# Optimization experiments

Measured on AMD Instinct MI355X. Metric: run time of the kernel, lower is better.

## Reference

```python
import jax, jax.numpy as jnp
import numpy as np

N_AGENTS = 32
STATE_DIM = 6 * N_AGENTS      # 192
CONTROL_DIM = 3 * N_AGENTS    # 96
HIDDEN = 100
NEWTON_ITERS = 40

# Index maps from the cvxpy objective:
#   p[u_x_r]^T u[u_idx] + p[u_y_r]^T u[2*u_idx] + p[u_z_r]^T u[3*u_idx]
_u_idx = np.arange(N_AGENTS)
P_IDX = np.concatenate([3 * np.arange(1, N_AGENTS + 1),
                        4 * np.arange(1, N_AGENTS + 1),
                        5 * np.arange(1, N_AGENTS + 1)])
U_IDX = np.concatenate([_u_idx, 2 * _u_idx, 3 * _u_idx])


def _p_net(t, z, W1, b1, W2, b2, W3, b3):
    # DefaultPNet: MLP on concat([t, z]) with tanh hiddens (hidden_dim=100)
    x = jnp.concatenate([t, z], axis=-1)          # [B, 1+STATE_DIM]
    h = jnp.tanh(x @ W1 + b1)
    h = jnp.tanh(h @ W2 + b2)
    return h @ W3 + b3                            # [B, STATE_DIM]


def _solve_qp(q):
    # min_u q^T u + 0.5||u||^2 + 0.25||u||^4  (unconstrained, strictly convex)
    # Stationarity: q + (1+||u||^2) u = 0 => u = -q/(1+s), s = ||u||^2
    # => s (1+s)^2 = ||q||^2 ; solve scalar cubic per row via Newton.
    r = jnp.sum(q * q, axis=-1)                   # [B]
    s0 = jnp.cbrt(r)                              # good init: s ~ r^(1/3) for large r

    def step(s, _):
        one = 1.0 + s
        f = s * one * one - r
        fp = one * one + 2.0 * s * one
        return jnp.maximum(s - f / fp, 0.0), None

    s, _ = jax.lax.scan(step, s0, None, length=NEWTON_ITERS)
    return -q / (1.0 + s)[:, None]                # [B, CONTROL_DIM]


def setup_inputs() -> dict:
    key = jax.random.key(0)
    ks = jax.random.split(key, 8)
    B = 131072
    in_dim = 1 + STATE_DIM
    sc1 = 1.0 / np.sqrt(in_dim)
    sc2 = 1.0 / np.sqrt(HIDDEN)
    return {
        "z": jax.random.normal(ks[0], (B, STATE_DIM), jnp.float32),
        "t": jax.random.uniform(ks[1], (B, 1), jnp.float32),
        "W1": jax.random.normal(ks[2], (in_dim, HIDDEN), jnp.float32) * sc1,
        "b1": jnp.zeros((HIDDEN,), jnp.float32),
        "W2": jax.random.normal(ks[3], (HIDDEN, HIDDEN), jnp.float32) * sc2,
        "b2": jnp.zeros((HIDDEN,), jnp.float32),
        "W3": jax.random.normal(ks[4], (HIDDEN, STATE_DIM), jnp.float32) * sc2,
        "b3": jnp.zeros((STATE_DIM,), jnp.float32),
    }


def reference(z, t, W1, b1, W2, b2, W3, b3):
    p = _p_net(t, z, W1, b1, W2, b2, W3, b3)      # [B, STATE_DIM]
    # Accumulate linear coefficients onto u (indices overlap, so scatter-add)
    q = jnp.zeros((p.shape[0], CONTROL_DIM), p.dtype).at[:, U_IDX].add(p[:, P_IDX])
    return _solve_qp(q)                            # ustar [B, CONTROL_DIM]
```

## Files before the change

kernel.cpp:

```cpp
#include <hip/hip_runtime.h>
#include <hip/hip_bf16.h>


typedef __attribute__((ext_vector_type(8))) short short8;
typedef __attribute__((ext_vector_type(4))) short short4v;
typedef __attribute__((ext_vector_type(4))) float f32x4;

#define HST 116

__device__ __forceinline__ unsigned short f2bf(float f) {
  unsigned u = __float_as_uint(f);
  u += 0x7fffu + ((u >> 16) & 1u);
  return (unsigned short)(u >> 16);
}
__device__ __forceinline__ float tanh_fast(float x) {
  float ax = fabsf(x);
  float e = __builtin_amdgcn_exp2f(ax * -2.88539008177792681f);
  float r = (1.f - e) * __builtin_amdgcn_rcpf(1.f + e);
  return copysignf(r, x);
}

__global__ void cvx_prep(const float* __restrict__ W1, const float* __restrict__ b1,
                         const float* __restrict__ W2, const float* __restrict__ b2,
                         const float* __restrict__ W3, const float* __restrict__ b3,
                         short* __restrict__ pw) {
  int idx = blockIdx.x * 256 + threadIdx.x;

  if (idx < 21504) {
    int kt = idx / 3584, rem = idx % 3584;
    int nt = rem / 512, e = rem % 512;
    int lane = e >> 3, j = e & 7;
    int k = kt * 32 + (lane >> 4) * 8 + j;
    int n = nt * 16 + (lane & 15);
    float wv = (n < 100) ? W1[(k + 1) * 100 + n] : 0.f;
    pw[(kt * 7 + nt) * 512 + e] = (short)f2bf(wv);
    return;
  }
  idx -= 21504;
  if (idx < 14336) {
    int kt = idx / 3584, rem = idx % 3584;
    int nt = rem / 512, e = rem % 512;
    int lane = e >> 3, j = e & 7;
    int k = kt * 32 + (lane >> 4) * 8 + j;
    int n = nt * 16 + (lane & 15);
    float wv = (k < 100 && n < 100) ? W2[k * 100 + n] : 0.f;
    pw[21504 + (kt * 7 + nt) * 512 + e] = (short)f2bf(wv);
    return;
  }
  idx -= 14336;
  if (idx < 12288) {
    int kt = idx / 3072, rem = idx % 3072;
    int nt = rem / 512, e = rem % 512;
    int lane = e >> 3, j = e & 7;
    int k = kt * 32 + (lane >> 4) * 8 + j;
    int u = nt * 16 + (lane & 15);
    float wv = 0.f;
    if (k < 100) {
      const float* wr = W3 + k * 192;
      if (u <= 31) wv += wr[3 * u + 3];
      if ((u & 1) == 0 && u <= 62) wv += wr[2 * u + 4];
      if (u % 3 == 0 && u <= 93) wv += wr[(5 * u) / 3 + 5];
    }
    pw[35840 + (kt * 6 + nt) * 512 + e] = (short)f2bf(wv);
    return;
  }
  idx -= 12288;
  float* cb = (float*)(pw + 48128);
  if (idx < 112) { cb[idx] = (idx < 100) ? W1[idx] : 0.f; return; }
  idx -= 112;
  if (idx < 112) { cb[112 + idx] = (idx < 100) ? b1[idx] : 0.f; return; }
  idx -= 112;
  if (idx < 112) { cb[224 + idx] = (idx < 100) ? b2[idx] : 0.f; return; }
  idx -= 112;
  if (idx < 96) {
    int u = idx;
    float v = 0.f;
    if (u <= 31) v += b3[3 * u + 3];
    if ((u & 1) == 0 && u <= 62) v += b3[2 * u + 4];
    if (u % 3 == 0 && u <= 93) v += b3[(5 * u) / 3 + 5];
    cb[336 + u] = v;
  }
}

__global__ __launch_bounds__(512, 2) void cvx_main(
    const float* __restrict__ zin, const float* __restrict__ tin,
    const short* __restrict__ pw, float* __restrict__ out) {
  __shared__ __align__(16) short wbuf[48128];
  __shared__ __align__(16) short hbuf[8 * 32 * HST];

  const int tid = threadIdx.x;
  const int wid = tid >> 6;
  const int lane = tid & 63;
  const int l15 = lane & 15;
  const int qd = lane >> 4;

  for (int f = wid; f < 94; f += 8) {
    const short* g = pw + f * 512 + lane * 8;
    __builtin_amdgcn_global_load_lds(
        (const __attribute__((address_space(1))) void*)g,
        (__attribute__((address_space(3))) void*)&wbuf[f * 512], 16, 0, 0);
  }

  const float* cb = (const float*)(pw + 48128);
  float w0v[7], b1v[7], b2v[7], bqv[6];
#pragma unroll
  for (int nt = 0; nt < 7; nt++) {
    w0v[nt] = cb[nt * 16 + l15];
    b1v[nt] = cb[112 + nt * 16 + l15];
    b2v[nt] = cb[224 + nt * 16 + l15];
  }
#pragma unroll
  for (int nt = 0; nt < 6; nt++) bqv[nt] = cb[336 + nt * 16 + l15];

  const int row0 = blockIdx.x * 512 + wid * 32;
  const int hb = wid * 32 * HST;

  f32x4 zc[2][6][2];
  float tc[2];
#pragma unroll
  for (int mt = 0; mt < 2; mt++) {
    const float* zr = zin + (size_t)(row0 + mt * 16 + l15) * 192 + qd * 8;
#pragma unroll
    for (int kt = 0; kt < 6; kt++) {
      zc[mt][kt][0] = *(const f32x4*)(zr + kt * 32);
      zc[mt][kt][1] = *(const f32x4*)(zr + kt * 32 + 4);
    }
    tc[mt] = tin[row0 + mt * 16 + l15];
  }

  __syncthreads();

  auto ldh = [&](int off) -> short8 {
    short4v a = *(const short4v*)&hbuf[off];
    short4v b = *(const short4v*)&hbuf[off + 4];
    return __builtin_shufflevector(a, b, 0, 1, 2, 3, 4, 5, 6, 7);
  };

#pragma unroll 1
  for (int it = 0; it < 2; ++it) {
    const int rb = row0 + it * 256;

    short8 XA[2][6];
#pragma unroll
    for (int mt = 0; mt < 2; mt++)
#pragma unroll
      for (int kt = 0; kt < 6; kt++) {
        union { short8 s; __hip_bfloat162 h[4]; } u;
        f32x4 a = zc[mt][kt][0], b = zc[mt][kt][1];
        u.h[0] = __float22bfloat162_rn(make_float2(a[0], a[1]));
        u.h[1] = __float22bfloat162_rn(make_float2(a[2], a[3]));
        u.h[2] = __float22bfloat162_rn(make_float2(b[0], b[1]));
        u.h[3] = __float22bfloat162_rn(make_float2(b[2], b[3]));
        XA[mt][kt] = u.s;
      }
    float tv0 = tc[0], tv1 = tc[1];

    if (it == 0) {
#pragma unroll
      for (int mt = 0; mt < 2; mt++) {
        const float* zr = zin + (size_t)(row0 + 256 + mt * 16 + l15) * 192 + qd * 8;
#pragma unroll
        for (int kt = 0; kt < 6; kt++) {
          zc[mt][kt][0] = *(const f32x4*)(zr + kt * 32);
          zc[mt][kt][1] = *(const f32x4*)(zr + kt * 32 + 4);
        }
        tc[mt] = tin[row0 + 256 + mt * 16 + l15];
      }
    }

    f32x4 acc[2][7];
#pragma unroll
    for (int nt = 0; nt < 7; nt++) {
      f32x4 zzz = {0.f, 0.f, 0.f, 0.f};
      acc[0][nt] = zzz; acc[1][nt] = zzz;
    }
#pragma unroll
    for (int kt = 0; kt < 6; kt++)
#pragma unroll
      for (int nt = 0; nt < 7; nt++) {
        short8 bf = *(const short8*)&wbuf[(kt * 7 + nt) * 512 + lane * 8];
        acc[0][nt] = __builtin_amdgcn_mfma_f32_16x16x32_bf16(XA[0][kt], bf, acc[0][nt], 0, 0, 0);
        acc[1][nt] = __builtin_amdgcn_mfma_f32_16x16x32_bf16(XA[1][kt], bf, acc[1][nt], 0, 0, 0);
      }
    float tr[2][4];
#pragma unroll
    for (int r = 0; r < 4; r++) {
      tr[0][r] = __shfl(tv0, qd * 4 + r);
      tr[1][r] = __shfl(tv1, qd * 4 + r);
    }
#pragma unroll
    for (int mt = 0; mt < 2; mt++)
#pragma unroll
      for (int nt = 0; nt < 7; nt++)
#pragma unroll
        for (int r = 0; r < 4; r++) {
          float v = fmaf(tr[mt][r], w0v[nt], acc[mt][nt][r] + b1v[nt]);
          hbuf[hb + (mt * 16 + qd * 4 + r) * HST + nt * 16 + l15] = (short)f2bf(tanh_fast(v));
        }

    short8 HA[2][4];
#pragma unroll
    for (int mt = 0; mt < 2; mt++) {
      int ro = hb + (mt * 16 + l15) * HST;
#pragma unroll
      for (int kt = 0; kt < 3; kt++) HA[mt][kt] = ldh(ro + kt * 32 + qd * 8);
      HA[mt][3] = ldh(ro + 96 + (qd & 1) * 8);
    }
#pragma unroll
    for (int nt = 0; nt < 7; nt++) {
      f32x4 zzz = {0.f, 0.f, 0.f, 0.f};
      acc[0][nt] = zzz; acc[1][nt] = zzz;
    }
#pragma unroll
    for (int kt = 0; kt < 4; kt++)
#pragma unroll
      for (int nt = 0; nt < 7; nt++) {
        short8 bf = *(const short8*)&wbuf[(42 + kt * 7 + nt) * 512 + lane * 8];
        acc[0][nt] = __builtin_amdgcn_mfma_f32_16x16x32_bf16(HA[0][kt], bf, acc[0][nt], 0, 0, 0);
        acc[1][nt] = __builtin_amdgcn_mfma_f32_16x16x32_bf16(HA[1][kt], bf, acc[1][nt], 0, 0, 0);
      }
#pragma unroll
    for (int mt = 0; mt < 2; mt++)
#pragma unroll
      for (int nt = 0; nt < 7; nt++)
#pragma unroll
        for (int r = 0; r < 4; r++) {
          float v = acc[mt][nt][r] + b2v[nt];
          hbuf[hb + (mt * 16 + qd * 4 + r) * HST + nt * 16 + l15] = (short)f2bf(tanh_fast(v));
        }

#pragma unroll
    for (int mt = 0; mt < 2; mt++) {
      int ro = hb + (mt * 16 + l15) * HST;
#pragma unroll
      for (int kt = 0; kt < 3; kt++) HA[mt][kt] = ldh(ro + kt * 32 + qd * 8);
      HA[mt][3] = ldh(ro + 96 + (qd & 1) * 8);
    }
    f32x4 qa[2][6];
#pragma unroll
    for (int nt = 0; nt < 6; nt++) {
      f32x4 zzz = {0.f, 0.f, 0.f, 0.f};
      qa[0][nt] = zzz; qa[1][nt] = zzz;
    }
#pragma unroll
    for (int kt = 0; kt < 4; kt++)
#pragma unroll
      for (int nt = 0; nt < 6; nt++) {
        short8 bf = *(const short8*)&wbuf[(70 + kt * 6 + nt) * 512 + lane * 8];
        qa[0][nt] = __builtin_amdgcn_mfma_f32_16x16x32_bf16(HA[0][kt], bf, qa[0][nt], 0, 0, 0);
        qa[1][nt] = __builtin_amdgcn_mfma_f32_16x16x32_bf16(HA[1][kt], bf, qa[1][nt], 0, 0, 0);
      }

#pragma unroll
    for (int mt = 0; mt < 2; mt++) {
#pragma unroll
      for (int nt = 0; nt < 6; nt++) {
        float bq = bqv[nt];
        qa[mt][nt][0] += bq; qa[mt][nt][1] += bq;
        qa[mt][nt][2] += bq; qa[mt][nt][3] += bq;
      }
      f32x4 rs = {0.f, 0.f, 0.f, 0.f};
#pragma unroll
      for (int nt = 0; nt < 6; nt++) rs += qa[mt][nt] * qa[mt][nt];
      float rv[4];
#pragma unroll
      for (int r = 0; r < 4; r++) {
        float v = rs[r];
        v += __shfl_xor(v, 1);
        v += __shfl_xor(v, 2);
        v += __shfl_xor(v, 4);
        v += __shfl_xor(v, 8);
        rv[r] = v;
      }
      float r2 = rv[l15 & 3];
      float s = __builtin_amdgcn_exp2f(__builtin_amdgcn_logf(r2) * 0.333333333333f);
#pragma unroll
      for (int itn = 0; itn < 8; itn++) {
        float one = 1.f + s;
        float fv = fmaf(s * one, one, -r2);
        float fp = one * fmaf(2.f, s, one);
        s = fmaxf(s - fv * __builtin_amdgcn_rcpf(fp), 0.f);
      }
      float myinv = -__builtin_amdgcn_rcpf(1.f + s);
#pragma unroll
      for (int r = 0; r < 4; r++) {
        float inv = __shfl(myinv, (lane & 48) | r);
        float* orow = out + (size_t)(rb + mt * 16 + qd * 4 + r) * 96;
#pragma unroll
        for (int nt = 0; nt < 6; nt++)
          orow[nt * 16 + l15] = qa[mt][nt][r] * inv;
      }
    }
  }
}

extern "C" void kernel_launch(void* const* d_in, const int* in_sizes, int n_in,
                              void* d_out, int out_size, void* d_ws, size_t ws_size,
                              hipStream_t stream) {
  const float* z  = (const float*)d_in[0];
  const float* t  = (const float*)d_in[1];
  const float* W1 = (const float*)d_in[2];
  const float* b1 = (const float*)d_in[3];
  const float* W2 = (const float*)d_in[4];
  const float* b2 = (const float*)d_in[5];
  const float* W3 = (const float*)d_in[6];
  const float* b3 = (const float*)d_in[7];
  float* out = (float*)d_out;
  int B = in_sizes[0] / 192;

  short* pw = (short*)d_ws;
  cvx_prep<<<190, 256, 0, stream>>>(W1, b1, W2, b2, W3, b3, pw);
  cvx_main<<<B / 512, 512, 0, stream>>>(z, t, pw, out);
}
```

Before: 192.8 us.

## Halve rows per wave and double block size to 1024 threads

Each wave now processes one 16-row M tile per iteration instead of two. The block doubles to 16 waves, so each block still covers 512 rows. Bias and W1 time-column vectors move from per-lane registers into a shared LDS array. The aim is to cut register pressure and put more waves on each CU to hide MFMA, LDS and global latency. The cost is that every weight fragment read from LDS now feeds one MFMA instead of two, which doubles LDS weight traffic per unit of work.

```diff
diff --git a/kernel.cpp b/kernel.cpp
--- a/kernel.cpp
+++ b/kernel.cpp
@@ -82,11 +82,12 @@
   }
 }
 
-__global__ __launch_bounds__(512, 2) void cvx_main(
+__global__ __launch_bounds__(1024, 4) void cvx_main(
     const float* __restrict__ zin, const float* __restrict__ tin,
     const short* __restrict__ pw, float* __restrict__ out) {
   __shared__ __align__(16) short wbuf[48128];
-  __shared__ __align__(16) short hbuf[8 * 32 * HST];
+  __shared__ __align__(16) short hbuf[16 * 16 * HST];
+  __shared__ __align__(16) float cbs[436];
 
   const int tid = threadIdx.x;
   const int wid = tid >> 6;
@@ -94,38 +95,27 @@
   const int l15 = lane & 15;
   const int qd = lane >> 4;
 
-  for (int f = wid; f < 94; f += 8) {
+  for (int f = wid; f < 94; f += 16) {
     const short* g = pw + f * 512 + lane * 8;
     __builtin_amdgcn_global_load_lds(
         (const __attribute__((address_space(1))) void*)g,
         (__attribute__((address_space(3))) void*)&wbuf[f * 512], 16, 0, 0);
   }
-
-  const float* cb = (const float*)(pw + 48128);
-  float w0v[7], b1v[7], b2v[7], bqv[6];
-#pragma unroll
-  for (int nt = 0; nt < 7; nt++) {
-    w0v[nt] = cb[nt * 16 + l15];
-    b1v[nt] = cb[112 + nt * 16 + l15];
-    b2v[nt] = cb[224 + nt * 16 + l15];
-  }
-#pragma unroll
-  for (int nt = 0; nt < 6; nt++) bqv[nt] = cb[336 + nt * 16 + l15];
-
-  const int row0 = blockIdx.x * 512 + wid * 32;
-  const int hb = wid * 32 * HST;
-
-  f32x4 zc[2][6][2];
-  float tc[2];
-#pragma unroll
-  for (int mt = 0; mt < 2; mt++) {
-    const float* zr = zin + (size_t)(row0 + mt * 16 + l15) * 192 + qd * 8;
+  if (tid < 436) cbs[tid] = ((const float*)(pw + 48128))[tid];
+
+  const int r0 = blockIdx.x * 512 + wid * 16;
+  const int hb = wid * 16 * HST;
+
+  f32x4 zc[6][2];
+  float tv;
+  {
+    const float* zr = zin + (size_t)(r0 + l15) * 192 + qd * 8;
 #pragma unroll
     for (int kt = 0; kt < 6; kt++) {
-      zc[mt][kt][0] = *(const f32x4*)(zr + kt * 32);
-      zc[mt][kt][1] = *(const f32x4*)(zr + kt * 32 + 4);
-    }
-    tc[mt] = tin[row0 + mt * 16 + l15];
+      zc[kt][0] = *(const f32x4*)(zr + kt * 32);
+      zc[kt][1] = *(const f32x4*)(zr + kt * 32 + 4);
+    }
+    tv = tin[r0 + l15];
   }
 
   __syncthreads();
@@ -138,158 +128,131 @@
 
 #pragma unroll 1
   for (int it = 0; it < 2; ++it) {
-    const int rb = row0 + it * 256;
-
-    short8 XA[2][6];
-#pragma unroll
-    for (int mt = 0; mt < 2; mt++)
+    const int rb = r0 + it * 256;
+
+    short8 XA[6];
+#pragma unroll
+    for (int kt = 0; kt < 6; kt++) {
+      union { short8 s; __hip_bfloat162 h[4]; } u;
+      f32x4 a = zc[kt][0], b = zc[kt][1];
+      u.h[0] = __float22bfloat162_rn(make_float2(a[0], a[1]));
+      u.h[1] = __float22bfloat162_rn(make_float2(a[2], a[3]));
+      u.h[2] = __float22bfloat162_rn(make_float2(b[0], b[1]));
+      u.h[3] = __float22bfloat162_rn(make_float2(b[2], b[3]));
+      XA[kt] = u.s;
+    }
+    const float tcur = tv;
+
+    if (it == 0) {
+      const float* zr = zin + (size_t)(rb + 256 + l15) * 192 + qd * 8;
 #pragma unroll
       for (int kt = 0; kt < 6; kt++) {
-        union { short8 s; __hip_bfloat162 h[4]; } u;
-        f32x4 a = zc[mt][kt][0], b = zc[mt][kt][1];
-        u.h[0] = __float22bfloat162_rn(make_float2(a[0], a[1]));
-        u.h[1] = __float22bfloat162_rn(make_float2(a[2], a[3]));
-        u.h[2] = __float22bfloat162_rn(make_float2(b[0], b[1]));
-        u.h[3] = __float22bfloat162_rn(make_float2(b[2], b[3]));
-        XA[mt][kt] = u.s;
-      }
-    float tv0 = tc[0], tv1 = tc[1];
-
-    if (it == 0) {
-#pragma unroll
-      for (int mt = 0; mt < 2; mt++) {
-        const float* zr = zin + (size_t)(row0 + 256 + mt * 16 + l15) * 192 + qd * 8;
-#pragma unroll
-        for (int kt = 0; kt < 6; kt++) {
-          zc[mt][kt][0] = *(const f32x4*)(zr + kt * 32);
-          zc[mt][kt][1] = *(const f32x4*)(zr + kt * 32 + 4);
-        }
-        tc[mt] = tin[row0 + 256 + mt * 16 + l15];
-      }
-    }
-
-    f32x4 acc[2][7];
-#pragma unroll
-    for (int nt = 0; nt < 7; nt++) {
-      f32x4 zzz = {0.f, 0.f, 0.f, 0.f};
-      acc[0][nt] = zzz; acc[1][nt] = zzz;
-    }
+        zc[kt][0] = *(const f32x4*)(zr + kt * 32);
+        zc[kt][1] = *(const f32x4*)(zr + kt * 32 + 4);
+      }
+      tv = tin[rb + 256 + l15];
+    }
+
+    f32x4 acc[7];
+#pragma unroll
+    for (int nt = 0; nt < 7; nt++) { f32x4 z4 = {0.f, 0.f, 0.f, 0.f}; acc[nt] = z4; }
 #pragma unroll
     for (int kt = 0; kt < 6; kt++)
 #pragma unroll
       for (int nt = 0; nt < 7; nt++) {
         short8 bf = *(const short8*)&wbuf[(kt * 7 + nt) * 512 + lane * 8];
-        acc[0][nt] = __builtin_amdgcn_mfma_f32_16x16x32_bf16(XA[0][kt], bf, acc[0][nt], 0, 0, 0);
-        acc[1][nt] = __builtin_amdgcn_mfma_f32_16x16x32_bf16(XA[1][kt], bf, acc[1][nt], 0, 0, 0);
-      }
-    float tr[2][4];
-#pragma unroll
-    for (int r = 0; r < 4; r++) {
-      tr[0][r] = __shfl(tv0, qd * 4 + r);
-      tr[1][r] = __shfl(tv1, qd * 4 + r);
-    }
-#pragma unroll
-    for (int mt = 0; mt < 2; mt++)
-#pragma unroll
-      for (int nt = 0; nt < 7; nt++)
-#pragma unroll
-        for (int r = 0; r < 4; r++) {
-          float v = fmaf(tr[mt][r], w0v[nt], acc[mt][nt][r] + b1v[nt]);
-          hbuf[hb + (mt * 16 + qd * 4 + r) * HST + nt * 16 + l15] = (short)f2bf(tanh_fast(v));
-        }
-
-    short8 HA[2][4];
-#pragma unroll
-    for (int mt = 0; mt < 2; mt++) {
-      int ro = hb + (mt * 16 + l15) * HST;
-#pragma unroll
-      for (int kt = 0; kt < 3; kt++) HA[mt][kt] = ldh(ro + kt * 32 + qd * 8);
-      HA[mt][3] = ldh(ro + 96 + (qd & 1) * 8);
-    }
+        acc[nt] = __builtin_amdgcn_mfma_f32_16x16x32_bf16(XA[kt], bf, acc[nt], 0, 0, 0);
+      }
+    float tr[4];
+#pragma unroll
+    for (int r = 0; r < 4; r++) tr[r] = __shfl(tcur, qd * 4 + r);
 #pragma unroll
     for (int nt = 0; nt < 7; nt++) {
-      f32x4 zzz = {0.f, 0.f, 0.f, 0.f};
-      acc[0][nt] = zzz; acc[1][nt] = zzz;
-    }
+      float w0n = cbs[nt * 16 + l15];
+      float b1n = cbs[112 + nt * 16 + l15];
+#pragma unroll
+      for (int r = 0; r < 4; r++) {
+        float v = fmaf(tr[r], w0n, acc[nt][r] + b1n);
+        hbuf[hb + (qd * 4 + r) * HST + nt * 16 + l15] = (short)f2bf(tanh_fast(v));
+      }
+    }
+
+    short8 HA[4];
+    {
+      int ro = hb + l15 * HST;
+#pragma unroll
+      for (int kt = 0; kt < 3; kt++) HA[kt] = ldh(ro + kt * 32 + qd * 8);
+      HA[3] = ldh(ro + 96 + (qd & 1) * 8);
+    }
+#pragma unroll
+    for (int nt = 0; nt < 7; nt++) { f32x4 z4 = {0.f, 0.f, 0.f, 0.f}; acc[nt] = z4; }
 #pragma unroll
     for (int kt = 0; kt < 4; kt++)
 #pragma unroll
       for (int nt = 0; nt < 7; nt++) {
         short8 bf = *(const short8*)&wbuf[(42 + kt * 7 + nt) * 512 + lane * 8];
-        acc[0][nt] = __builtin_amdgcn_mfma_f32_16x16x32_bf16(HA[0][kt], bf, acc[0][nt], 0, 0, 0);
-        acc[1][nt] = __builtin_amdgcn_mfma_f32_16x16x32_bf16(HA[1][kt], bf, acc[1][nt], 0, 0, 0);
-      }
-#pragma unroll
-    for (int mt = 0; mt < 2; mt++)
-#pragma unroll
-      for (int nt = 0; nt < 7; nt++)
-#pragma unroll
-        for (int r = 0; r < 4; r++) {
-          float v = acc[mt][nt][r] + b2v[nt];
-          hbuf[hb + (mt * 16 + qd * 4 + r) * HST + nt * 16 + l15] = (short)f2bf(tanh_fast(v));
-        }
-
-#pragma unroll
-    for (int mt = 0; mt < 2; mt++) {
-      int ro = hb + (mt * 16 + l15) * HST;
-#pragma unroll
-      for (int kt = 0; kt < 3; kt++) HA[mt][kt] = ldh(ro + kt * 32 + qd * 8);
-      HA[mt][3] = ldh(ro + 96 + (qd & 1) * 8);
-    }
-    f32x4 qa[2][6];
-#pragma unroll
-    for (int nt = 0; nt < 6; nt++) {
-      f32x4 zzz = {0.f, 0.f, 0.f, 0.f};
-      qa[0][nt] = zzz; qa[1][nt] = zzz;
-    }
+        acc[nt] = __builtin_amdgcn_mfma_f32_16x16x32_bf16(HA[kt], bf, acc[nt], 0, 0, 0);
+      }
+#pragma unroll
+    for (int nt = 0; nt < 7; nt++) {
+      float b2n = cbs[224 + nt * 16 + l15];
+#pragma unroll
+      for (int r = 0; r < 4; r++)
+        hbuf[hb + (qd * 4 + r) * HST + nt * 16 + l15] = (short)f2bf(tanh_fast(acc[nt][r] + b2n));
+    }
+
+    {
+      int ro = hb + l15 * HST;
+#pragma unroll
+      for (int kt = 0; kt < 3; kt++) HA[kt] = ldh(ro + kt * 32 + qd * 8);
+      HA[3] = ldh(ro + 96 + (qd & 1) * 8);
+    }
+    f32x4 qa[6];
+#pragma unroll
+    for (int nt = 0; nt < 6; nt++) { f32x4 z4 = {0.f, 0.f, 0.f, 0.f}; qa[nt] = z4; }
 #pragma unroll
     for (int kt = 0; kt < 4; kt++)
 #pragma unroll
       for (int nt = 0; nt < 6; nt++) {
         short8 bf = *(const short8*)&wbuf[(70 + kt * 6 + nt) * 512 + lane * 8];
-        qa[0][nt] = __builtin_amdgcn_mfma_f32_16x16x32_bf16(HA[0][kt], bf, qa[0][nt], 0, 0, 0);
-        qa[1][nt] = __builtin_amdgcn_mfma_f32_16x16x32_bf16(HA[1][kt], bf, qa[1][nt], 0, 0, 0);
-      }
-
-#pragma unroll
-    for (int mt = 0; mt < 2; mt++) {
-#pragma unroll
-      for (int nt = 0; nt < 6; nt++) {
-        float bq = bqv[nt];
-        qa[mt][nt][0] += bq; qa[mt][nt][1] += bq;
-        qa[mt][nt][2] += bq; qa[mt][nt][3] += bq;
-      }
-      f32x4 rs = {0.f, 0.f, 0.f, 0.f};
-#pragma unroll
-      for (int nt = 0; nt < 6; nt++) rs += qa[mt][nt] * qa[mt][nt];
-      float rv[4];
-#pragma unroll
-      for (int r = 0; r < 4; r++) {
-        float v = rs[r];
-        v += __shfl_xor(v, 1);
-        v += __shfl_xor(v, 2);
-        v += __shfl_xor(v, 4);
-        v += __shfl_xor(v, 8);
-        rv[r] = v;
-      }
-      float r2 = rv[l15 & 3];
-      float s = __builtin_amdgcn_exp2f(__builtin_amdgcn_logf(r2) * 0.333333333333f);
-#pragma unroll
-      for (int itn = 0; itn < 8; itn++) {
-        float one = 1.f + s;
-        float fv = fmaf(s * one, one, -r2);
-        float fp = one * fmaf(2.f, s, one);
-        s = fmaxf(s - fv * __builtin_amdgcn_rcpf(fp), 0.f);
-      }
-      float myinv = -__builtin_amdgcn_rcpf(1.f + s);
-#pragma unroll
-      for (int r = 0; r < 4; r++) {
-        float inv = __shfl(myinv, (lane & 48) | r);
-        float* orow = out + (size_t)(rb + mt * 16 + qd * 4 + r) * 96;
-#pragma unroll
-        for (int nt = 0; nt < 6; nt++)
-          orow[nt * 16 + l15] = qa[mt][nt][r] * inv;
-      }
+        qa[nt] = __builtin_amdgcn_mfma_f32_16x16x32_bf16(HA[kt], bf, qa[nt], 0, 0, 0);
+      }
+
+#pragma unroll
+    for (int nt = 0; nt < 6; nt++) {
+      float bq = cbs[336 + nt * 16 + l15];
+      qa[nt][0] += bq; qa[nt][1] += bq; qa[nt][2] += bq; qa[nt][3] += bq;
+    }
+    f32x4 rs = {0.f, 0.f, 0.f, 0.f};
+#pragma unroll
+    for (int nt = 0; nt < 6; nt++) rs += qa[nt] * qa[nt];
+    float rv[4];
+#pragma unroll
+    for (int r = 0; r < 4; r++) {
+      float v = rs[r];
+      v += __shfl_xor(v, 1);
+      v += __shfl_xor(v, 2);
+      v += __shfl_xor(v, 4);
+      v += __shfl_xor(v, 8);
+      rv[r] = v;
+    }
+    float r2 = rv[l15 & 3];
+    float s = __builtin_amdgcn_exp2f(__builtin_amdgcn_logf(r2) * 0.333333333333f);
+#pragma unroll
+    for (int itn = 0; itn < 8; itn++) {
+      float one = 1.f + s;
+      float fv = fmaf(s * one, one, -r2);
+      float fp = one * fmaf(2.f, s, one);
+      s = fmaxf(s - fv * __builtin_amdgcn_rcpf(fp), 0.f);
+    }
+    float myinv = -__builtin_amdgcn_rcpf(1.f + s);
+#pragma unroll
+    for (int r = 0; r < 4; r++) {
+      float inv = __shfl(myinv, (lane & 48) | r);
+      float* orow = out + (size_t)(rb + qd * 4 + r) * 96;
+#pragma unroll
+      for (int nt = 0; nt < 6; nt++)
+        orow[nt * 16 + l15] = qa[nt][r] * inv;
     }
   }
 }
@@ -310,5 +273,5 @@
 
   short* pw = (short*)d_ws;
   cvx_prep<<<190, 256, 0, stream>>>(W1, b1, W2, b2, W3, b3, pw);
-  cvx_main<<<B / 512, 512, 0, stream>>>(z, t, pw, out);
-}
+  cvx_main<<<B / 512, 1024, 0, stream>>>(z, t, pw, out);
+}
```

New measurement: 271.9 us. +41.1%, slower.
